# Kernel optimization log

Hardware: AMD Instinct MI355X
Metric: run time of the kernel (lower is better)

The kernel has to match this reference:

```python
import jax, jax.numpy as jnp
import numpy as np

N_EL, N_NB, DIM = 8192, 24, 256
CUTOFF = 5.0
F0, F1 = 32, 16
N_ENV = 8
N_FEAT = 4  # [dist, dx, dy, dz]


def setup_inputs() -> dict:
    key = jax.random.key(0)
    ks = jax.random.split(key, 24)
    d = {}
    d['elec'] = jax.random.normal(ks[0], (N_EL, DIM), jnp.float32)
    d['msg'] = jax.random.normal(ks[1], (N_EL, DIM), jnp.float32)
    # positions inside a box of half the cutoff so pairs are within range
    d['r'] = jax.random.uniform(ks[2], (N_EL, 3), jnp.float32) * (0.5 * CUTOFF)
    d['r_nb'] = jax.random.uniform(ks[3], (N_EL, N_NB, 3), jnp.float32) * (0.5 * CUTOFF)
    d['s'] = jax.random.randint(ks[4], (N_EL,), 0, 2, jnp.int32)
    d['s_nb'] = jax.random.randint(ks[5], (N_EL, N_NB), 0, 2, jnp.int32)
    d['hinit_nb'] = jax.random.normal(ks[6], (N_EL, N_NB, DIM), jnp.float32)
    # parameters
    def lecun(k, shape):
        fan_in = shape[0]
        return jax.random.normal(k, shape, jnp.float32) / np.float32(np.sqrt(fan_in))
    d['W_in'] = lecun(ks[7], (DIM, DIM)); d['b_in'] = jnp.zeros((DIM,), jnp.float32)
    d['ee_scales'] = jax.random.uniform(ks[8], (N_ENV,), jnp.float32, 0.5, CUTOFF)
    d['ee_kernel'] = lecun(ks[9], (N_FEAT, F0))
    d['ee_bias'] = 2.0 * jax.random.normal(ks[10], (F0,), jnp.float32)
    d['Wf'] = lecun(ks[11], (F0 + N_ENV, F1)); d['bf'] = jnp.zeros((F1,), jnp.float32)
    d['Wsame'] = lecun(ks[12], (F1, DIM))
    d['Wdiff'] = lecun(ks[13], (F1, DIM))
    d['W1'] = lecun(ks[14], (DIM, DIM)); d['b1'] = jnp.zeros((DIM,), jnp.float32)
    d['W2'] = lecun(ks[15], (DIM, DIM)); d['b2'] = jnp.zeros((DIM,), jnp.float32)
    d['W3'] = lecun(ks[16], (DIM, DIM)); d['b3'] = jnp.zeros((DIM,), jnp.float32)
    d['scale'] = jnp.float32(1.0)  # FixedScalingFactor (identity at init)
    return d


def _forward(elec, msg, r, r_nb, s, s_nb, hinit_nb,
             W_in, b_in, ee_scales, ee_kernel, ee_bias, Wf, bf,
             Wsame, Wdiff, W1, b1, W2, b2, W3, b3, scale):
    silu = jax.nn.silu
    elec1 = silu(elec @ W_in + b_in)                       # [N, D]
    # get_diff_features: [dist, dx, dy, dz]
    diff = r_nb - r[:, None, :]                             # [N, K, 3]
    dist = jnp.sqrt(jnp.sum(diff * diff, -1) + 1e-12)       # [N, K]
    feats = jnp.concatenate([dist[..., None], diff], -1)    # [N, K, 4]
    spin_mask = s[:, None] == s_nb                          # [N, K]
    # PairwiseFilter: MLP on diff-features + radial envelopes, smooth cutoff
    env = jnp.exp(-jnp.square(dist[..., None] / ee_scales)) # [N, K, E]
    h = silu(feats @ ee_kernel + ee_bias)                   # [N, K, F0]
    h = jnp.concatenate([h, env], -1)                       # [N, K, F0+E]
    x = dist / CUTOFF
    cut = jnp.where(dist < CUTOFF, jnp.square(1.0 - x) * (1.0 + 2.0 * x), 0.0)
    beta = (h @ Wf + bf) * cut[..., None]                   # [N, K, F1]
    gamma = jnp.where(spin_mask[..., None], beta @ Wsame, beta @ Wdiff)  # [N, K, D]
    hinit_msg = jnp.einsum('nid,nid->nd', silu(elec1[:, None] + hinit_nb), gamma)
    out = silu(elec1 @ W1 + b1 + hinit_msg)
    out = silu(out @ W2 + b2 + msg)
    out = silu(out @ W3 + b3)
    return (out + elec1) * scale


def reference(elec, msg, r, r_nb, s, s_nb, hinit_nb,
              W_in, b_in, ee_scales, ee_kernel, ee_bias, Wf, bf,
              Wsame, Wdiff, W1, b1, W2, b2, W3, b3, scale):
    return _forward(elec, msg, r, r_nb, s, s_nb, hinit_nb,
                    W_in, b_in, ee_scales, ee_kernel, ee_bias, Wf, bf,
                    Wsame, Wdiff, W1, b1, W2, b2, W3, b3, scale)
```

## Files before the change

kernel.cpp:

```cpp
#include <hip/hip_runtime.h>

#define DIM 256
#define PDIM 260
#define PD2  264
#define SBPITCH 20
#define NNB 24
#define NEL 8192
#define ROWS 16
#define NT 512
#define CUTOFF 5.0f
#define E1_OFF 524288

typedef unsigned int u32;
typedef unsigned short u16;
typedef __attribute__((ext_vector_type(8))) short bf16x8;
typedef __attribute__((ext_vector_type(4))) float f32x4;

#define GL_LDS(g, l) __builtin_amdgcn_global_load_lds( \
    (const __attribute__((address_space(1))) void*)(g), \
    (__attribute__((address_space(3))) void*)(l), 16, 0, 0)

__device__ __forceinline__ u16 f2b(float f){
  union{float f;u32 i;}v; v.f=f;
  u32 r = v.i + 0x7fffu + ((v.i>>16)&1u);
  return (u16)(r>>16);
}
__device__ __forceinline__ float b2f(u16 u){
  union{u32 i;float f;}v; v.i = ((u32)u)<<16; return v.f;
}
__device__ __forceinline__ float fast_silu(float x){
  float e = __builtin_amdgcn_exp2f(-1.44269504088896340f * x);
  return x * __builtin_amdgcn_rcpf(1.0f + e);
}

__global__ __launch_bounds__(256)
void wprep(const float* __restrict__ W0, const float* __restrict__ W1,
           const float* __restrict__ W2, const float* __restrict__ W3,
           const float* __restrict__ Wsame, const float* __restrict__ Wdiff,
           u16* __restrict__ ws){
  if (blockIdx.x < 1024){
    const int mat = blockIdx.x >> 8;
    const int n   = blockIdx.x & 255;
    const int k   = threadIdx.x;
    const float* W = (mat==0)?W0:(mat==1)?W1:(mat==2)?W2:W3;
    ws[(mat<<16) + (n<<8) + k] = f2b(W[(k<<8) + n]);
  } else {
    const int n = threadIdx.x;
    u16* dst = ws + 4*65536 + n*32;
    #pragma unroll
    for (int kk = 0; kk < 16; kk++){
      dst[kk]    = f2b(Wsame[kk*DIM + n]);
      dst[16+kk] = f2b(Wdiff[kk*DIM + n]);
    }
  }
}

template<int MODE, int ABF16>
__device__ __forceinline__ void gemm_mfma(
    const void* A, u16* sE1b, float* sR1,
    const u16* __restrict__ Wt, const float* __restrict__ bias,
    const float* __restrict__ extraGbl, float* __restrict__ outGbl,
    float scl, int n0, int t)
{
  const int lane = t & 63;
  const int ln   = lane & 15;
  const int quad = lane >> 4;
  const int nt0  = (t >> 6) << 1;
  f32x4 acc0 = {0.f,0.f,0.f,0.f};
  f32x4 acc1 = {0.f,0.f,0.f,0.f};
  const u16* bp0 = Wt + (nt0*16 + ln)*DIM;
  const u16* bp1 = bp0 + 16*DIM;
  #pragma unroll
  for (int ks = 0; ks < 8; ks++){
    const int k0 = ks*32 + quad*8;
    bf16x8 af;
    if (ABF16){
      af = *(const bf16x8*)((const u16*)A + ln*PD2 + k0);
    } else {
      const float* arow = (const float*)A + ln*PDIM;
      float4 a01 = *(const float4*)(arow + k0);
      float4 a23 = *(const float4*)(arow + k0 + 4);
      af[0]=(short)f2b(a01.x); af[1]=(short)f2b(a01.y);
      af[2]=(short)f2b(a01.z); af[3]=(short)f2b(a01.w);
      af[4]=(short)f2b(a23.x); af[5]=(short)f2b(a23.y);
      af[6]=(short)f2b(a23.z); af[7]=(short)f2b(a23.w);
    }
    bf16x8 b0 = *(const bf16x8*)(bp0 + k0);
    bf16x8 b1 = *(const bf16x8*)(bp1 + k0);
    acc0 = __builtin_amdgcn_mfma_f32_16x16x32_bf16(af, b0, acc0, 0, 0, 0);
    acc1 = __builtin_amdgcn_mfma_f32_16x16x32_bf16(af, b1, acc1, 0, 0, 0);
  }
  if (MODE == 2) __syncthreads();
  #pragma unroll
  for (int r = 0; r < 4; r++){
    const int m = quad*4 + r;
    #pragma unroll
    for (int tt = 0; tt < 2; tt++){
      const int n = (nt0+tt)*16 + ln;
      float v = (tt ? acc1[r] : acc0[r]) + bias[n];
      if (MODE == 2) v += extraGbl[(size_t)(n0+m)*DIM + n];
      v = fast_silu(v);
      if (MODE == 3) outGbl[(size_t)(n0+m)*DIM + n] = (v + b2f(sE1b[m*PD2 + n])) * scl;
      else           sR1[m*PDIM + n] = v;
    }
  }
}

__global__ __launch_bounds__(NT, 8)
void k1_gemm1(const float* __restrict__ elec, const float* __restrict__ bin,
              const u16* __restrict__ Wt, u16* __restrict__ elec1g)
{
  const int t  = threadIdx.x;
  const int n0 = blockIdx.x * ROWS;
  const int lane = t & 63;
  const int ln   = lane & 15;
  const int quad = lane >> 4;
  const int nt0  = (t >> 6) << 1;
  f32x4 acc0 = {0.f,0.f,0.f,0.f};
  f32x4 acc1 = {0.f,0.f,0.f,0.f};
  const u16* bp0 = Wt + (nt0*16 + ln)*DIM;
  const u16* bp1 = bp0 + 16*DIM;
  const float* arow = elec + (size_t)(n0 + ln)*DIM;
  #pragma unroll
  for (int ks = 0; ks < 8; ks++){
    const int k0 = ks*32 + quad*8;
    float4 a01 = *(const float4*)(arow + k0);
    float4 a23 = *(const float4*)(arow + k0 + 4);
    bf16x8 af;
    af[0]=(short)f2b(a01.x); af[1]=(short)f2b(a01.y);
    af[2]=(short)f2b(a01.z); af[3]=(short)f2b(a01.w);
    af[4]=(short)f2b(a23.x); af[5]=(short)f2b(a23.y);
    af[6]=(short)f2b(a23.z); af[7]=(short)f2b(a23.w);
    bf16x8 b0 = *(const bf16x8*)(bp0 + k0);
    bf16x8 b1 = *(const bf16x8*)(bp1 + k0);
    acc0 = __builtin_amdgcn_mfma_f32_16x16x32_bf16(af, b0, acc0, 0, 0, 0);
    acc1 = __builtin_amdgcn_mfma_f32_16x16x32_bf16(af, b1, acc1, 0, 0, 0);
  }
  #pragma unroll
  for (int r = 0; r < 4; r++){
    const int m = quad*4 + r;
    #pragma unroll
    for (int tt = 0; tt < 2; tt++){
      const int n = (nt0+tt)*16 + ln;
      float v = fast_silu((tt ? acc1[r] : acc0[r]) + bin[n]);
      elec1g[(size_t)(n0+m)*DIM + n] = f2b(v);
    }
  }
}

__global__ __launch_bounds__(NT, 4)
void k2_msg(const float* __restrict__ rpos, const float* __restrict__ rnb,
            const int* __restrict__ s, const int* __restrict__ snb,
            const float* __restrict__ hinit,
            const float* __restrict__ eesc, const float* __restrict__ eek,
            const float* __restrict__ eeb,  const float* __restrict__ Wf,
            const float* __restrict__ bfb,
            const u16* __restrict__ Wt, const u16* __restrict__ elec1g,
            float* __restrict__ hmsg)
{
  __shared__ u16   sBC[NNB*16*SBPITCH];
  __shared__ u32   sMaskB[ROWS];
  __shared__ float sH[8][2][512];
  __shared__ float sPar[824];
  const int t  = threadIdx.x;
  const int n0 = blockIdx.x * ROWS;
  const int lane = t & 63;
  const int w    = t >> 6;
  const int C0   = w << 5;

  const float* hsrc = hinit
      + (size_t)(n0 + (lane & 15)) * NNB * DIM + C0 + ((lane >> 4) << 2);
  float* sHw0 = &sH[w][0][0];
  float* sHw1 = &sH[w][1][0];
  GL_LDS(hsrc + 0*DIM,      sHw0);
  GL_LDS(hsrc + 0*DIM + 16, sHw0 + 256);
  GL_LDS(hsrc + 1*DIM,      sHw1);
  GL_LDS(hsrc + 1*DIM + 16, sHw1 + 256);

  if (t < ROWS) sMaskB[t] = 0u;
  for (int i = t; i < 824; i += NT){
    float v;
    if (i < 640)      v = Wf[i];
    else if (i < 768) v = eek[i-640];
    else if (i < 800) v = eeb[i-768];
    else if (i < 816) v = bfb[i-800];
    else              v = eesc[i-816];
    sPar[i] = v;
  }
  __syncthreads();

  if (t < ROWS*NNB) {
    const int rr = t / NNB;
    const int k  = t - rr*NNB;
    const int n  = n0 + rr;
    const float* rp  = rpos + n*3;
    const float* rnp = rnb + (n*NNB + k)*3;
    float dx = rnp[0] - rp[0];
    float dy = rnp[1] - rp[1];
    float dz = rnp[2] - rp[2];
    float dist = sqrtf(dx*dx + dy*dy + dz*dz + 1e-12f);
    float feats[4] = {dist, dx, dy, dz};
    float h[32];
    #pragma unroll
    for (int f4 = 0; f4 < 8; f4++){
      float4 a4 = *(const float4*)&sPar[768 + 4*f4];
      float av[4] = {a4.x, a4.y, a4.z, a4.w};
      #pragma unroll
      for (int i = 0; i < 4; i++){
        float4 kv = *(const float4*)&sPar[640 + i*32 + 4*f4];
        av[0]+=feats[i]*kv.x; av[1]+=feats[i]*kv.y; av[2]+=feats[i]*kv.z; av[3]+=feats[i]*kv.w;
      }
      h[4*f4+0]=fast_silu(av[0]); h[4*f4+1]=fast_silu(av[1]);
      h[4*f4+2]=fast_silu(av[2]); h[4*f4+3]=fast_silu(av[3]);
    }
    float env[8];
    #pragma unroll
    for (int e = 0; e < 8; e++){
      float q = dist * __builtin_amdgcn_rcpf(sPar[816 + e]);
      env[e] = __builtin_amdgcn_exp2f(-1.44269504088896340f * q * q);
    }
    float xx = dist * (1.0f/CUTOFF);
    float cut = (dist < CUTOFF) ? (1.0f-xx)*(1.0f-xx)*(1.0f+2.0f*xx) : 0.0f;
    u16* rowp = &sBC[(k*16 + rr)*SBPITCH];
    #pragma unroll
    for (int j4 = 0; j4 < 4; j4++){
      float4 a4 = *(const float4*)&sPar[800 + 4*j4];
      float av[4] = {a4.x, a4.y, a4.z, a4.w};
      #pragma unroll
      for (int f = 0; f < 40; f++){
        float val = (f < 32) ? h[f] : env[f-32];
        float4 wv = *(const float4*)&sPar[f*16 + 4*j4];
        av[0]+=val*wv.x; av[1]+=val*wv.y; av[2]+=val*wv.z; av[3]+=val*wv.w;
      }
      ushort4 bv;
      bv.x = f2b(av[0]*cut); bv.y = f2b(av[1]*cut);
      bv.z = f2b(av[2]*cut); bv.w = f2b(av[3]*cut);
      *(ushort4*)(rowp + 4*j4) = bv;
    }
    if (s[n] == snb[n*NNB + k]) atomicOr(&sMaskB[rr], 1u << k);
  }
  __syncthreads();

  {
    const int ln   = lane & 15;
    const int quad = lane >> 4;
    const int nA   = C0 + (quad << 2);
    const u16* Wcat = Wt + 4*65536;
    bf16x8 bs0 = *(const bf16x8*)(Wcat + (C0 + ln)*32 + quad*8);
    bf16x8 bs1 = *(const bf16x8*)(Wcat + (C0 + 16 + ln)*32 + quad*8);

    float e1A[4], e1B[4];
    {
      ushort4 ea = *(const ushort4*)&elec1g[(size_t)(n0+ln)*DIM + nA];
      ushort4 eb = *(const ushort4*)&elec1g[(size_t)(n0+ln)*DIM + nA + 16];
      e1A[0]=b2f(ea.x); e1A[1]=b2f(ea.y); e1A[2]=b2f(ea.z); e1A[3]=b2f(ea.w);
      e1B[0]=b2f(eb.x); e1B[1]=b2f(eb.y); e1B[2]=b2f(eb.z); e1B[3]=b2f(eb.w);
    }
    const u32 mb = sMaskB[ln];
    float hmA[4] = {0.f,0.f,0.f,0.f};
    float hmB[4] = {0.f,0.f,0.f,0.f};
    for (int k = 0; k < NNB; k++){
      if (k < NNB-1) { asm volatile("s_waitcnt vmcnt(2)" ::: "memory"); }
      else           { asm volatile("s_waitcnt vmcnt(0)" ::: "memory"); }
      float* sHw = (k & 1) ? sHw1 : sHw0;
      float4 hv0 = *(const float4*)&sHw[lane*4];
      float4 hv1 = *(const float4*)&sHw[256 + lane*4];
      bf16x8 b8 = *(const bf16x8*)(&sBC[(k*16 + ln)*SBPITCH + (quad&1)*8]);
      const u16 km = (u16)((((u32)(quad>>1) ^ ((mb>>k)&1u)) != 0u) ? 0xFFFFu : 0u);
      bf16x8 af;
      #pragma unroll
      for (int j = 0; j < 8; j++) af[j] = (short)((u16)b8[j] & km);
      __builtin_amdgcn_sched_barrier(0);
      if (k + 2 < NNB){
        GL_LDS(hsrc + (size_t)(k+2)*DIM,      sHw);
        GL_LDS(hsrc + (size_t)(k+2)*DIM + 16, sHw + 256);
      }
      f32x4 z = {0.f,0.f,0.f,0.f};
      f32x4 g0 = __builtin_amdgcn_mfma_f32_16x16x32_bf16(bs0, af, z, 0, 0, 0);
      f32x4 g1 = __builtin_amdgcn_mfma_f32_16x16x32_bf16(bs1, af, z, 0, 0, 0);
      hmA[0] += fast_silu(e1A[0]+hv0.x)*g0[0];
      hmA[1] += fast_silu(e1A[1]+hv0.y)*g0[1];
      hmA[2] += fast_silu(e1A[2]+hv0.z)*g0[2];
      hmA[3] += fast_silu(e1A[3]+hv0.w)*g0[3];
      hmB[0] += fast_silu(e1B[0]+hv1.x)*g1[0];
      hmB[1] += fast_silu(e1B[1]+hv1.y)*g1[1];
      hmB[2] += fast_silu(e1B[2]+hv1.z)*g1[2];
      hmB[3] += fast_silu(e1B[3]+hv1.w)*g1[3];
    }
    *(float4*)&hmsg[(size_t)(n0+ln)*DIM + nA]      = make_float4(hmA[0],hmA[1],hmA[2],hmA[3]);
    *(float4*)&hmsg[(size_t)(n0+ln)*DIM + nA + 16] = make_float4(hmB[0],hmB[1],hmB[2],hmB[3]);
  }
}

__global__ __launch_bounds__(NT, 8)
void k3_gemms(const float* __restrict__ msg, const u16* __restrict__ elec1g,
              const float* __restrict__ b1, const float* __restrict__ b2,
              const float* __restrict__ b3, const float* __restrict__ scalep,
              const u16* __restrict__ Wt, float* __restrict__ out)
{
  __shared__ float sR1[ROWS*PDIM];
  __shared__ u16   sE1b[ROWS*PD2];
  const int t  = threadIdx.x;
  const int n0 = blockIdx.x * ROWS;

  {
    const u32* e1u = (const u32*)elec1g;
    #pragma unroll
    for (int h = 0; h < 8; h++){
      const int i   = t + h*NT;
      const int row = i >> 7;
      const int c2  = i & 127;
      *(u32*)&sE1b[row*PD2 + 2*c2] = e1u[(size_t)(n0+row)*128 + c2];
    }
  }
  __syncthreads();

  const float scl = scalep[0];
  gemm_mfma<2,1>(sE1b, sE1b, sR1, Wt + (1<<16), b1, out, nullptr, 0.f, n0, t);
  __syncthreads();
  gemm_mfma<2,0>(sR1, sE1b, sR1, Wt + (2<<16), b2, msg, nullptr, 0.f, n0, t);
  __syncthreads();
  gemm_mfma<3,0>(sR1, sE1b, sR1, Wt + (3<<16), b3, nullptr, out, scl, n0, t);
}

extern "C" void kernel_launch(void* const* d_in, const int* in_sizes, int n_in,
                              void* d_out, int out_size, void* d_ws, size_t ws_size,
                              hipStream_t stream) {
  (void)in_sizes; (void)n_in; (void)ws_size; (void)out_size;
  const float* elec  = (const float*)d_in[0];
  const float* msg   = (const float*)d_in[1];
  const float* rpos  = (const float*)d_in[2];
  const float* rnb   = (const float*)d_in[3];
  const int*   s     = (const int*)d_in[4];
  const int*   snb   = (const int*)d_in[5];
  const float* hinit = (const float*)d_in[6];
  const float* Win   = (const float*)d_in[7];
  const float* bin   = (const float*)d_in[8];
  const float* eesc  = (const float*)d_in[9];
  const float* eek   = (const float*)d_in[10];
  const float* eeb   = (const float*)d_in[11];
  const float* Wf    = (const float*)d_in[12];
  const float* bfb   = (const float*)d_in[13];
  const float* Wsame = (const float*)d_in[14];
  const float* Wdiff = (const float*)d_in[15];
  const float* W1    = (const float*)d_in[16];
  const float* b1    = (const float*)d_in[17];
  const float* W2    = (const float*)d_in[18];
  const float* b2    = (const float*)d_in[19];
  const float* W3    = (const float*)d_in[20];
  const float* b3    = (const float*)d_in[21];
  const float* scl   = (const float*)d_in[22];
  float* outp        = (float*)d_out;
  u16*   wt          = (u16*)d_ws;
  u16*   elec1g      = wt + E1_OFF;

  wprep<<<dim3(1025), dim3(256), 0, stream>>>(Win, W1, W2, W3, Wsame, Wdiff, wt);
  k1_gemm1<<<dim3(NEL/ROWS), dim3(NT), 0, stream>>>(elec, bin, wt, elec1g);
  k2_msg<<<dim3(NEL/ROWS), dim3(NT), 0, stream>>>(
      rpos, rnb, s, snb, hinit, eesc, eek, eeb, Wf, bfb, wt, elec1g, outp);
  k3_gemms<<<dim3(NEL/ROWS), dim3(NT), 0, stream>>>(
      msg, elec1g, b1, b2, b3, scl, wt, outp);
}
```

Baseline: 396.8 us.

## Restructure message kernel to one electron per block with VALU gamma

The message kernel now runs one block of 256 threads per electron instead of one 512-thread block per 16 electrons. Each wave loads six neighbour rows of hinit straight into registers, replacing the async LDS double-buffered pipeline. Gamma is computed with scalar FMAs from bf16 Wsame/Wdiff staged in LDS rather than with MFMA, and partial sums are reduced across waves through shared memory. The trade is more parallelism and simpler loads against redundant per-block weight staging, 16x more blocks, and more VALU work.

Measured after the change: 434.8 us. 1.1x slower.

```diff
diff --git a/kernel.cpp b/kernel.cpp
--- a/kernel.cpp
+++ b/kernel.cpp
@@ -3,22 +3,18 @@
 #define DIM 256
 #define PDIM 260
 #define PD2  264
-#define SBPITCH 20
 #define NNB 24
 #define NEL 8192
 #define ROWS 16
 #define NT 512
 #define CUTOFF 5.0f
 #define E1_OFF 524288
+#define SWP 264
 
 typedef unsigned int u32;
 typedef unsigned short u16;
 typedef __attribute__((ext_vector_type(8))) short bf16x8;
 typedef __attribute__((ext_vector_type(4))) float f32x4;
-
-#define GL_LDS(g, l) __builtin_amdgcn_global_load_lds( \
-    (const __attribute__((address_space(1))) void*)(g), \
-    (__attribute__((address_space(3))) void*)(l), 16, 0, 0)
 
 __device__ __forceinline__ u16 f2b(float f){
   union{float f;u32 i;}v; v.f=f;
@@ -148,37 +144,50 @@
   }
 }
 
-__global__ __launch_bounds__(NT, 4)
+__global__ __launch_bounds__(256, 4)
 void k2_msg(const float* __restrict__ rpos, const float* __restrict__ rnb,
             const int* __restrict__ s, const int* __restrict__ snb,
             const float* __restrict__ hinit,
             const float* __restrict__ eesc, const float* __restrict__ eek,
             const float* __restrict__ eeb,  const float* __restrict__ Wf,
             const float* __restrict__ bfb,
-            const u16* __restrict__ Wt, const u16* __restrict__ elec1g,
-            float* __restrict__ hmsg)
+            const float* __restrict__ Wsame, const float* __restrict__ Wdiff,
+            const u16* __restrict__ elec1g, float* __restrict__ hmsg)
 {
-  __shared__ u16   sBC[NNB*16*SBPITCH];
-  __shared__ u32   sMaskB[ROWS];
-  __shared__ float sH[8][2][512];
+  __shared__ u16   sWb[32*SWP];
   __shared__ float sPar[824];
-  const int t  = threadIdx.x;
-  const int n0 = blockIdx.x * ROWS;
+  __shared__ float sBeta[NNB*16];
+  __shared__ float sRed[4][260];
+  __shared__ u32   sMask0;
+  const int t    = threadIdx.x;
+  const int n    = blockIdx.x;
+  const int w    = t >> 6;
   const int lane = t & 63;
-  const int w    = t >> 6;
-  const int C0   = w << 5;
-
-  const float* hsrc = hinit
-      + (size_t)(n0 + (lane & 15)) * NNB * DIM + C0 + ((lane >> 4) << 2);
-  float* sHw0 = &sH[w][0][0];
-  float* sHw1 = &sH[w][1][0];
-  GL_LDS(hsrc + 0*DIM,      sHw0);
-  GL_LDS(hsrc + 0*DIM + 16, sHw0 + 256);
-  GL_LDS(hsrc + 1*DIM,      sHw1);
-  GL_LDS(hsrc + 1*DIM + 16, sHw1 + 256);
-
-  if (t < ROWS) sMaskB[t] = 0u;
-  for (int i = t; i < 824; i += NT){
+  const int c0   = lane << 2;
+
+  ushort4 e1u = *(const ushort4*)(elec1g + (size_t)n*DIM + c0);
+  const float* hp = hinit + ((size_t)n*NNB + w*6)*DIM + c0;
+  float4 h0 = *(const float4*)(hp + 0*DIM);
+  float4 h1 = *(const float4*)(hp + 1*DIM);
+  float4 h2 = *(const float4*)(hp + 2*DIM);
+  float4 h3 = *(const float4*)(hp + 3*DIM);
+  float4 h4 = *(const float4*)(hp + 4*DIM);
+  float4 h5 = *(const float4*)(hp + 5*DIM);
+  __builtin_amdgcn_sched_barrier(0);
+
+  if (t == 0) sMask0 = 0u;
+  #pragma unroll
+  for (int it = 0; it < 8; it++){
+    const int i = t + it*256;
+    const int r  = i >> 6;
+    const int c4 = (i & 63) << 2;
+    const float* Wsrc = (r < 16) ? (Wsame + r*DIM + c4) : (Wdiff + (r-16)*DIM + c4);
+    float4 v = *(const float4*)Wsrc;
+    ushort4 b;
+    b.x=f2b(v.x); b.y=f2b(v.y); b.z=f2b(v.z); b.w=f2b(v.w);
+    *(ushort4*)&sWb[r*SWP + c4] = b;
+  }
+  for (int i = t; i < 824; i += 256){
     float v;
     if (i < 640)      v = Wf[i];
     else if (i < 768) v = eek[i-640];
@@ -189,12 +198,11 @@
   }
   __syncthreads();
 
-  if (t < ROWS*NNB) {
-    const int rr = t / NNB;
-    const int k  = t - rr*NNB;
-    const int n  = n0 + rr;
+  if (t < 4*NNB) {
+    const int pr = t >> 2;
+    const int j4 = t & 3;
     const float* rp  = rpos + n*3;
-    const float* rnp = rnb + (n*NNB + k)*3;
+    const float* rnp = rnb + (n*NNB + pr)*3;
     float dx = rnp[0] - rp[0];
     float dy = rnp[1] - rp[1];
     float dz = rnp[2] - rp[2];
@@ -221,74 +229,57 @@
     }
     float xx = dist * (1.0f/CUTOFF);
     float cut = (dist < CUTOFF) ? (1.0f-xx)*(1.0f-xx)*(1.0f+2.0f*xx) : 0.0f;
-    u16* rowp = &sBC[(k*16 + rr)*SBPITCH];
-    #pragma unroll
-    for (int j4 = 0; j4 < 4; j4++){
-      float4 a4 = *(const float4*)&sPar[800 + 4*j4];
-      float av[4] = {a4.x, a4.y, a4.z, a4.w};
-      #pragma unroll
-      for (int f = 0; f < 40; f++){
-        float val = (f < 32) ? h[f] : env[f-32];
-        float4 wv = *(const float4*)&sPar[f*16 + 4*j4];
-        av[0]+=val*wv.x; av[1]+=val*wv.y; av[2]+=val*wv.z; av[3]+=val*wv.w;
-      }
-      ushort4 bv;
-      bv.x = f2b(av[0]*cut); bv.y = f2b(av[1]*cut);
-      bv.z = f2b(av[2]*cut); bv.w = f2b(av[3]*cut);
-      *(ushort4*)(rowp + 4*j4) = bv;
-    }
-    if (s[n] == snb[n*NNB + k]) atomicOr(&sMaskB[rr], 1u << k);
-  }
-  __syncthreads();
-
+    float4 a4 = *(const float4*)&sPar[800 + 4*j4];
+    float av[4] = {a4.x, a4.y, a4.z, a4.w};
+    #pragma unroll
+    for (int f = 0; f < 40; f++){
+      float val = (f < 32) ? h[f] : env[f-32];
+      float4 wv = *(const float4*)&sPar[f*16 + 4*j4];
+      av[0]+=val*wv.x; av[1]+=val*wv.y; av[2]+=val*wv.z; av[3]+=val*wv.w;
+    }
+    *(float4*)&sBeta[pr*16 + j4*4] =
+        make_float4(av[0]*cut, av[1]*cut, av[2]*cut, av[3]*cut);
+    if (j4 == 0 && s[n] == snb[n*NNB + pr]) atomicOr(&sMask0, 1u << pr);
+  }
+  __syncthreads();
+
+  const u32 mb = sMask0;
+  float g[6][4];
+  #pragma unroll
+  for (int i = 0; i < 6; i++){ g[i][0]=0.f; g[i][1]=0.f; g[i][2]=0.f; g[i][3]=0.f; }
+  for (int j = 0; j < 16; j++){
+    ushort4 su = *(const ushort4*)&sWb[j*SWP + c0];
+    ushort4 du = *(const ushort4*)&sWb[(j+16)*SWP + c0];
+    float ws0=b2f(su.x), ws1=b2f(su.y), ws2=b2f(su.z), ws3=b2f(su.w);
+    float wd0=b2f(du.x), wd1=b2f(du.y), wd2=b2f(du.z), wd3=b2f(du.w);
+    #pragma unroll
+    for (int i = 0; i < 6; i++){
+      const int k = w*6 + i;
+      const float b = sBeta[k*16 + j];
+      const bool m = ((mb >> k) & 1u) != 0u;
+      g[i][0] += b * (m ? ws0 : wd0);
+      g[i][1] += b * (m ? ws1 : wd1);
+      g[i][2] += b * (m ? ws2 : wd2);
+      g[i][3] += b * (m ? ws3 : wd3);
+    }
+  }
+
+  float e0=b2f(e1u.x), e1=b2f(e1u.y), e2=b2f(e1u.z), e3=b2f(e1u.w);
+  float hm0=0.f, hm1=0.f, hm2=0.f, hm3=0.f;
+#define CONSUME(i, hv) \
+  hm0 += fast_silu(e0 + hv.x) * g[i][0]; \
+  hm1 += fast_silu(e1 + hv.y) * g[i][1]; \
+  hm2 += fast_silu(e2 + hv.z) * g[i][2]; \
+  hm3 += fast_silu(e3 + hv.w) * g[i][3];
+  CONSUME(0, h0) CONSUME(1, h1) CONSUME(2, h2)
+  CONSUME(3, h3) CONSUME(4, h4) CONSUME(5, h5)
+#undef CONSUME
+
+  *(float4*)&sRed[w][c0] = make_float4(hm0, hm1, hm2, hm3);
+  __syncthreads();
   {
-    const int ln   = lane & 15;
-    const int quad = lane >> 4;
-    const int nA   = C0 + (quad << 2);
-    const u16* Wcat = Wt + 4*65536;
-    bf16x8 bs0 = *(const bf16x8*)(Wcat + (C0 + ln)*32 + quad*8);
-    bf16x8 bs1 = *(const bf16x8*)(Wcat + (C0 + 16 + ln)*32 + quad*8);
-
-    float e1A[4], e1B[4];
-    {
-      ushort4 ea = *(const ushort4*)&elec1g[(size_t)(n0+ln)*DIM + nA];
-      ushort4 eb = *(const ushort4*)&elec1g[(size_t)(n0+ln)*DIM + nA + 16];
-      e1A[0]=b2f(ea.x); e1A[1]=b2f(ea.y); e1A[2]=b2f(ea.z); e1A[3]=b2f(ea.w);
-      e1B[0]=b2f(eb.x); e1B[1]=b2f(eb.y); e1B[2]=b2f(eb.z); e1B[3]=b2f(eb.w);
-    }
-    const u32 mb = sMaskB[ln];
-    float hmA[4] = {0.f,0.f,0.f,0.f};
-    float hmB[4] = {0.f,0.f,0.f,0.f};
-    for (int k = 0; k < NNB; k++){
-      if (k < NNB-1) { asm volatile("s_waitcnt vmcnt(2)" ::: "memory"); }
-      else           { asm volatile("s_waitcnt vmcnt(0)" ::: "memory"); }
-      float* sHw = (k & 1) ? sHw1 : sHw0;
-      float4 hv0 = *(const float4*)&sHw[lane*4];
-      float4 hv1 = *(const float4*)&sHw[256 + lane*4];
-      bf16x8 b8 = *(const bf16x8*)(&sBC[(k*16 + ln)*SBPITCH + (quad&1)*8]);
-      const u16 km = (u16)((((u32)(quad>>1) ^ ((mb>>k)&1u)) != 0u) ? 0xFFFFu : 0u);
-      bf16x8 af;
-      #pragma unroll
-      for (int j = 0; j < 8; j++) af[j] = (short)((u16)b8[j] & km);
-      __builtin_amdgcn_sched_barrier(0);
-      if (k + 2 < NNB){
-        GL_LDS(hsrc + (size_t)(k+2)*DIM,      sHw);
-        GL_LDS(hsrc + (size_t)(k+2)*DIM + 16, sHw + 256);
-      }
-      f32x4 z = {0.f,0.f,0.f,0.f};
-      f32x4 g0 = __builtin_amdgcn_mfma_f32_16x16x32_bf16(bs0, af, z, 0, 0, 0);
-      f32x4 g1 = __builtin_amdgcn_mfma_f32_16x16x32_bf16(bs1, af, z, 0, 0, 0);
-      hmA[0] += fast_silu(e1A[0]+hv0.x)*g0[0];
-      hmA[1] += fast_silu(e1A[1]+hv0.y)*g0[1];
-      hmA[2] += fast_silu(e1A[2]+hv0.z)*g0[2];
-      hmA[3] += fast_silu(e1A[3]+hv0.w)*g0[3];
-      hmB[0] += fast_silu(e1B[0]+hv1.x)*g1[0];
-      hmB[1] += fast_silu(e1B[1]+hv1.y)*g1[1];
-      hmB[2] += fast_silu(e1B[2]+hv1.z)*g1[2];
-      hmB[3] += fast_silu(e1B[3]+hv1.w)*g1[3];
-    }
-    *(float4*)&hmsg[(size_t)(n0+ln)*DIM + nA]      = make_float4(hmA[0],hmA[1],hmA[2],hmA[3]);
-    *(float4*)&hmsg[(size_t)(n0+ln)*DIM + nA + 16] = make_float4(hmB[0],hmB[1],hmB[2],hmB[3]);
+    float r = sRed[0][t] + sRed[1][t] + sRed[2][t] + sRed[3][t];
+    hmsg[(size_t)n*DIM + t] = r;
   }
 }
 
@@ -356,8 +347,9 @@
 
   wprep<<<dim3(1025), dim3(256), 0, stream>>>(Win, W1, W2, W3, Wsame, Wdiff, wt);
   k1_gemm1<<<dim3(NEL/ROWS), dim3(NT), 0, stream>>>(elec, bin, wt, elec1g);
-  k2_msg<<<dim3(NEL/ROWS), dim3(NT), 0, stream>>>(
-      rpos, rnb, s, snb, hinit, eesc, eek, eeb, Wf, bfb, wt, elec1g, outp);
+  k2_msg<<<dim3(NEL), dim3(256), 0, stream>>>(
+      rpos, rnb, s, snb, hinit, eesc, eek, eeb, Wf, bfb,
+      Wsame, Wdiff, elec1g, outp);
   k3_gemms<<<dim3(NEL/ROWS), dim3(NT), 0, stream>>>(
       msg, elec1g, b1, b2, b3, scl, wt, outp);
 }
```
